# Kernel tuning notes

Hardware: AMD Instinct MI355X
Metric: run time of the kernel (lower is better)

Reference implementation:

```python
import jax, jax.numpy as jnp
import numpy as np

WS = 7            # window_size
HEADS = 12
HEAD_DIM = 32
DIM = 384
INNER = HEADS * HEAD_DIM
DISP = WS // 2    # displacement for shifted windows


def _rel_indices():
    idx = np.array([[x, y] for x in range(WS) for y in range(WS)])  # (49,2)
    d = idx[None, :, :] - idx[:, None, :] + WS - 1                   # (49,49,2), values in [0, 2*WS-2]
    return d


def _masks():
    # upper/lower mask (applied to last row of windows)
    ul = np.zeros((WS * WS, WS * WS), np.float32)
    ul[-DISP * WS:, :-DISP * WS] = -np.inf
    ul[:-DISP * WS, -DISP * WS:] = -np.inf
    # left/right mask (applied to last column of windows)
    lr = np.zeros((WS, WS, WS, WS), np.float32)
    lr[:, -DISP:, :, :-DISP] = -np.inf
    lr[:, :-DISP, :, -DISP:] = -np.inf
    lr = lr.reshape(WS * WS, WS * WS)
    return ul, lr


_RI = _rel_indices()
_UL, _LR = _masks()


def setup_inputs() -> dict:
    key = jax.random.key(0)
    k1, k2, k3, k4, k5 = jax.random.split(key, 5)
    b, H, W = 32, 56, 56
    x = jax.random.normal(k1, (b, H, W, DIM), jnp.float32)
    w_qkv = jax.random.normal(k2, (DIM, 3 * INNER), jnp.float32) * (DIM ** -0.5)
    pos_emb = jax.random.normal(k3, (2 * WS - 1, 2 * WS - 1), jnp.float32)
    w_out = jax.random.normal(k4, (INNER, DIM), jnp.float32) * (INNER ** -0.5)
    b_out = jax.random.normal(k5, (DIM,), jnp.float32)
    return {"x": x, "w_qkv": w_qkv, "pos_emb": pos_emb, "w_out": w_out, "b_out": b_out}


def reference(x, w_qkv, pos_emb, w_out, b_out):
    b, H, W, _ = x.shape
    nwh, nww = H // WS, W // WS
    # cyclic shift
    x = jnp.roll(x, (-DISP, -DISP), (1, 2))
    qkv = x @ w_qkv                                     # [b,H,W,3*INNER]
    q, k, v = jnp.split(qkv, 3, axis=-1)

    def to_win(t):
        # [b,H,W,INNER] -> [b, heads, n_windows, WS*WS, head_dim]
        t = t.reshape(b, nwh, WS, nww, WS, HEADS, HEAD_DIM)
        return t.transpose(0, 5, 1, 3, 2, 4, 6).reshape(b, HEADS, nwh * nww, WS * WS, HEAD_DIM)

    q, k, v = map(to_win, (q, k, v))
    dots = jnp.einsum('bhwid,bhwjd->bhwij', q, k) * (HEAD_DIM ** -0.5)
    # relative position bias gather
    dots = dots + pos_emb[_RI[:, :, 0], _RI[:, :, 1]]
    # shifted-window masks: last row of windows and last column of windows
    dots = dots.at[:, :, -nww:].add(jnp.asarray(_UL))
    dots = dots.at[:, :, nww - 1::nww].add(jnp.asarray(_LR))
    attn = jax.nn.softmax(dots, axis=-1)
    out = jnp.einsum('bhwij,bhwjd->bhwid', attn, v)
    # windows back to image layout
    out = out.reshape(b, HEADS, nwh, nww, WS, WS, HEAD_DIM)
    out = out.transpose(0, 2, 4, 3, 5, 1, 6).reshape(b, H, W, INNER)
    out = out @ w_out + b_out
    return jnp.roll(out, (DISP, DISP), (1, 2))
```

## Files before the change

### kernel.cpp

```cpp
#include <hip/hip_runtime.h>

typedef __attribute__((ext_vector_type(8))) short short8;
typedef __attribute__((ext_vector_type(4))) int int4v;
typedef __attribute__((ext_vector_type(4))) float f32x4;

#define MFMA(a, b, c) __builtin_amdgcn_mfma_f32_16x16x32_bf16(a, b, c, 0, 0, 0)
#define SCALE 0.17677669529663687f

__device__ __forceinline__ short f2bf(float f) {
  union { float f; unsigned u; } v;
  v.f = f;
  unsigned r = v.u + 0x7fffu + ((v.u >> 16) & 1u);
  return (short)(r >> 16);
}

__device__ __forceinline__ unsigned cvt_pk(float lo, float hi) {
  unsigned r;
  asm("v_cvt_pk_bf16_f32 %0, %1, %2" : "=v"(r) : "v"(lo), "v"(hi));
  return r;
}

#define XS_STR 424
#define VT_OFF 0
#define Q_OFF  16384
#define K_OFF  28928
#define AO_STR 392

__global__ void prep_weights(const float* __restrict__ wqkv,
                             const float* __restrict__ wout,
                             short* __restrict__ wqkvT,
                             short* __restrict__ woutT) {
  int i = blockIdx.x * 256 + threadIdx.x;
  if (i < 1152 * 384) {
    int n = i / 384, k = i - (i / 384) * 384;
    float w = wqkv[k * 1152 + n];
    if (n < 384) w *= SCALE;
    wqkvT[i] = f2bf(w);
  }
  if (i < 384 * 384) {
    int n = i / 384, k = i - (i / 384) * 384;
    woutT[i] = f2bf(wout[k * 384 + n]);
  }
}

__global__ void prep_bias(const float* __restrict__ pe, float* __restrict__ btabT) {
  int id = blockIdx.x * 256 + threadIdx.x;
  if (id >= 16384) return;
  int t = id >> 12;
  int i = (id >> 6) & 63;
  int j = id & 63;
  float v;
  if (i < 49 && j < 49) {
    int ai = i / 7, bi = i - ai * 7, aj = j / 7, bj = j - aj * 7;
    v = pe[(aj - ai + 6) * 13 + (bj - bi + 6)];
    if ((t & 1) && ((i >= 28) != (j >= 28))) v = -1e30f;
    if ((t & 2) && ((bi >= 4) != (bj >= 4))) v = -1e30f;
  } else if (j < 49) {
    v = 0.f;
  } else {
    v = -1e30f;
  }
  btabT[((t * 64 + i) * 16 + (j & 15)) * 4 + (j >> 4)] = v;
}

#define GEMM_STEP(BUF)                                                        \
  {                                                                           \
    short8 a0 = *(const short8*)(pA[0] + k * 32);                             \
    short8 a1 = *(const short8*)(pA[1] + k * 32);                             \
    short8 a2 = *(const short8*)(pA[2] + k * 32);                             \
    short8 a3 = *(const short8*)(pA[3] + k * 32);                             \
    acc[0][0] = MFMA(a0, BUF[0], acc[0][0]);                                  \
    acc[1][0] = MFMA(a1, BUF[0], acc[1][0]);                                  \
    acc[2][0] = MFMA(a2, BUF[0], acc[2][0]);                                  \
    acc[3][0] = MFMA(a3, BUF[0], acc[3][0]);                                  \
    acc[0][1] = MFMA(a0, BUF[1], acc[0][1]);                                  \
    acc[1][1] = MFMA(a1, BUF[1], acc[1][1]);                                  \
    acc[2][1] = MFMA(a2, BUF[1], acc[2][1]);                                  \
    acc[3][1] = MFMA(a3, BUF[1], acc[3][1]);                                  \
    acc[0][2] = MFMA(a0, BUF[2], acc[0][2]);                                  \
    acc[1][2] = MFMA(a1, BUF[2], acc[1][2]);                                  \
    acc[2][2] = MFMA(a2, BUF[2], acc[2][2]);                                  \
    acc[3][2] = MFMA(a3, BUF[2], acc[3][2]);                                  \
  }

#define GEMM_PIPELINE()                                                       \
  _Pragma("unroll")                                                           \
  for (int n = 0; n < 3; ++n) bA[n] = *(const short8*)(pB[n]);                \
  _Pragma("unroll")                                                           \
  for (int n = 0; n < 3; ++n) bB[n] = *(const short8*)(pB[n] + 32);           \
  _Pragma("unroll")                                                           \
  for (int k = 0; k < 12; ++k) {                                              \
    if (k + 2 < 12) {                                                         \
      const int off = (k + 2) * 32;                                           \
      if (k % 3 == 0) {                                                       \
        _Pragma("unroll")                                                     \
        for (int n = 0; n < 3; ++n) bC[n] = *(const short8*)(pB[n] + off);    \
      } else if (k % 3 == 1) {                                                \
        _Pragma("unroll")                                                     \
        for (int n = 0; n < 3; ++n) bA[n] = *(const short8*)(pB[n] + off);    \
      } else {                                                                \
        _Pragma("unroll")                                                     \
        for (int n = 0; n < 3; ++n) bB[n] = *(const short8*)(pB[n] + off);    \
      }                                                                       \
    }                                                                         \
    if (k % 3 == 0) GEMM_STEP(bA)                                             \
    else if (k % 3 == 1) GEMM_STEP(bB)                                        \
    else GEMM_STEP(bC)                                                        \
  }

__global__ __launch_bounds__(512, 4) void swin_qkv_attn(
    const float* __restrict__ x, const short* __restrict__ wqkvT,
    const float* __restrict__ btabT, short* __restrict__ aout) {

  __shared__ short smemA[49 * XS_STR];
  char* smc = (char*)smemA;

  const int tid = threadIdx.x;
  const int lane = tid & 63;
  const int wv = tid >> 6;
  const int l15 = lane & 15;
  const int lhi = lane >> 4;

  const int bid = blockIdx.x;
  const int sw = (bid & 7) * 768 + (bid >> 3);
  const int g = sw - (sw / 3) * 3;
  const int bw = sw / 3;
  const int batch = bw >> 6;
  const int win = bw & 63;
  const int wy = win >> 3, wx = win & 7;

  const size_t xbase = (size_t)batch * (56 * 56 * 384);
  const f32x4 zf = {0.f, 0.f, 0.f, 0.f};

  {
    const int tok = tid >> 3;
    const int sub = tid & 7;
    if (tok < 49) {
      int iy = (tok * 37) >> 8;
      int ix = tok - iy * 7;
      int rr = wy * 7 + iy + 3; if (rr >= 56) rr -= 56;
      int cc = wx * 7 + ix + 3; if (cc >= 56) cc -= 56;
      const float* xp = x + xbase + (size_t)(rr * 56 + cc) * 384;
#pragma unroll
      for (int j = 0; j < 6; ++j) {
        const int c8 = (sub + 8 * j) * 8;
        const float4 fa = *(const float4*)(xp + c8);
        const float4 fb = *(const float4*)(xp + c8 + 4);
        int4v p;
        p.x = (int)cvt_pk(fa.x, fa.y);
        p.y = (int)cvt_pk(fa.z, fa.w);
        p.z = (int)cvt_pk(fb.x, fb.y);
        p.w = (int)cvt_pk(fb.z, fb.w);
        *(int4v*)(&smemA[tok * XS_STR + c8]) = p;
      }
    }
  }
  __syncthreads();

  f32x4 acc[4][3];
  const int n0 = wv * 48;
  {
    const short* pB[3];
#pragma unroll
    for (int n = 0; n < 3; ++n) {
      const int c0 = n0 + n * 16;
      const int seg = c0 >> 7;
      const int hloc = (c0 >> 5) & 3;
      const int wrow = seg * 384 + (g * 4 + hloc) * 32 + (c0 & 31);
      pB[n] = wqkvT + (size_t)(wrow + l15) * 384 + lhi * 8;
    }
#pragma unroll
    for (int m = 0; m < 4; ++m)
#pragma unroll
      for (int n = 0; n < 3; ++n) acc[m][n] = zf;

    const short* pA[4];
#pragma unroll
    for (int m = 0; m < 4; ++m) {
      int row = m * 16 + l15;
      int rc = row < 49 ? row : 48;
      pA[m] = &smemA[rc * XS_STR + lhi * 8];
    }

    short8 bA[3], bB[3], bC[3];
    GEMM_PIPELINE()
  }
  __syncthreads();

  {
#pragma unroll
    for (int n = 0; n < 3; ++n) {
      const int c0 = n0 + n * 16;
      if (c0 < 256) {
#pragma unroll
        for (int m = 0; m < 4; ++m)
#pragma unroll
          for (int r = 0; r < 4; ++r) {
            const int row = m * 16 + lhi * 4 + r;
            if (row < 49) {
              const int f = c0 + l15;
              const int base = (f < 128) ? Q_OFF : K_OFF;
              const int fo = (f & 127) * 2;
              *(short*)(smc + base + row * 256 + (fo ^ ((row & 7) << 4))) =
                  f2bf(acc[m][n][r]);
            }
          }
      } else {
        const int d = c0 - 256 + l15;
        char* vrow = smc + VT_OFF + d * 128;
        const int dx = (d & 7) << 4;
#pragma unroll
        for (int m = 0; m < 4; ++m)
#pragma unroll
          for (int r = 0; r < 4; r += 2) {
            const int row = m * 16 + lhi * 4 + r;
            const unsigned pk = cvt_pk(acc[m][n][r], acc[m][n][r + 1]);
            *(unsigned*)(vrow + ((2 * row) ^ dx)) = pk;
          }
      }
    }
  }
  __syncthreads();

  {
    const int hl = wv >> 1;
    const int mh = wv & 1;
    const int tt = (wy == 7 ? 1 : 0) | (wx == 7 ? 2 : 0);

    f32x4 bb[2][4];
#pragma unroll
    for (int mi = 0; mi < 2; ++mi)
#pragma unroll
      for (int r = 0; r < 4; ++r) {
        const int i = mh * 32 + mi * 16 + lhi * 4 + r;
        bb[mi][r] = *(const f32x4*)(&btabT[((tt * 64 + i) * 16 + l15) * 4]);
      }

    short8 qa[2];
#pragma unroll
    for (int mi = 0; mi < 2; ++mi) {
      int row = mh * 32 + mi * 16 + l15;
      int rc = row < 49 ? row : 48;
      qa[mi] = *(const short8*)(smc + Q_OFF + rc * 256 +
                                ((hl * 64 + lhi * 16) ^ ((rc & 7) << 4)));
    }
    f32x4 s[2][4];
#pragma unroll
    for (int nt = 0; nt < 4; ++nt) {
      int jr = nt * 16 + l15;
      int jc = jr < 49 ? jr : 48;
      short8 kb = *(const short8*)(smc + K_OFF + jc * 256 +
                                   ((hl * 64 + lhi * 16) ^ ((jc & 7) << 4)));
#pragma unroll
      for (int mi = 0; mi < 2; ++mi) s[mi][nt] = MFMA(qa[mi], kb, zf);
    }

#pragma unroll
    for (int mi = 0; mi < 2; ++mi)
#pragma unroll
      for (int r = 0; r < 4; ++r)
#pragma unroll
        for (int nt = 0; nt < 4; ++nt)
          s[mi][nt][r] += bb[mi][r][nt];

#pragma unroll
    for (int mi = 0; mi < 2; ++mi)
#pragma unroll
      for (int r = 0; r < 4; ++r) {
        float mx = fmaxf(fmaxf(s[mi][0][r], s[mi][1][r]),
                         fmaxf(s[mi][2][r], s[mi][3][r]));
        mx = fmaxf(mx, __shfl_xor(mx, 1));
        mx = fmaxf(mx, __shfl_xor(mx, 2));
        mx = fmaxf(mx, __shfl_xor(mx, 4));
        mx = fmaxf(mx, __shfl_xor(mx, 8));
        float p0 = __expf(s[mi][0][r] - mx);
        float p1 = __expf(s[mi][1][r] - mx);
        float p2 = __expf(s[mi][2][r] - mx);
        float p3 = __expf(s[mi][3][r] - mx);
        float sum = p0 + p1 + p2 + p3;
        sum += __shfl_xor(sum, 1);
        sum += __shfl_xor(sum, 2);
        sum += __shfl_xor(sum, 4);
        sum += __shfl_xor(sum, 8);
        const float inv = __builtin_amdgcn_rcpf(sum);
        s[mi][0][r] = p0 * inv;
        s[mi][1][r] = p1 * inv;
        s[mi][2][r] = p2 * inv;
        s[mi][3][r] = p3 * inv;
      }

    short8 vb[2][2];
#pragma unroll
    for (int ks = 0; ks < 2; ++ks)
#pragma unroll
      for (int n2 = 0; n2 < 2; ++n2) {
        const int dg = hl * 32 + n2 * 16 + l15;
        vb[ks][n2] = *(const short8*)(smc + VT_OFF + dg * 128 +
                                      ((ks * 64 + lhi * 16) ^ ((dg & 7) << 4)));
      }

    __syncthreads();

    char* Pb = smc + Q_OFF + wv * 2304;
    f32x4 O[2][2];
#pragma unroll
    for (int mi = 0; mi < 2; ++mi) {
#pragma unroll
      for (int r = 0; r < 4; ++r) {
        const int rowl = lhi * 4 + r;
        short* pr = (short*)(Pb + rowl * 144);
        pr[ 0 + l15] = f2bf(s[mi][0][r]);
        pr[16 + l15] = f2bf(s[mi][1][r]);
        pr[32 + l15] = f2bf(s[mi][2][r]);
        pr[48 + l15] = f2bf(s[mi][3][r]);
      }
      const short8 pa0 = *(const short8*)(Pb + l15 * 144 +  0 + lhi * 16);
      const short8 pa1 = *(const short8*)(Pb + l15 * 144 + 64 + lhi * 16);
      O[mi][0] = MFMA(pa0, vb[0][0], zf);
      O[mi][1] = MFMA(pa0, vb[0][1], zf);
      O[mi][0] = MFMA(pa1, vb[1][0], O[mi][0]);
      O[mi][1] = MFMA(pa1, vb[1][1], O[mi][1]);
    }

    short* ab = aout + (size_t)bw * (49 * 384) + (g * 4 + hl) * 32;
#pragma unroll
    for (int mi = 0; mi < 2; ++mi)
#pragma unroll
      for (int n2 = 0; n2 < 2; ++n2)
#pragma unroll
        for (int r = 0; r < 4; ++r) {
          int row = mh * 32 + mi * 16 + lhi * 4 + r;
          if (row < 49) ab[row * 384 + n2 * 16 + l15] = f2bf(O[mi][n2][r]);
        }
  }
}

__global__ __launch_bounds__(512, 4) void swin_outproj(
    const short* __restrict__ aout, const short* __restrict__ woutT,
    const float* __restrict__ bout, float* __restrict__ out) {

  __shared__ short ao[49 * AO_STR];

  const int tid = threadIdx.x;
  const int lane = tid & 63;
  const int wv = tid >> 6;
  const int l15 = lane & 15;
  const int lhi = lane >> 4;

  const int bw = blockIdx.x;
  const int batch = bw >> 6;
  const int win = bw & 63;
  const int wy = win >> 3, wx = win & 7;

  const size_t xbase = (size_t)batch * (56 * 56 * 384);
  const f32x4 zf = {0.f, 0.f, 0.f, 0.f};

  const short* abg = aout + (size_t)bw * (49 * 384);
  for (int t = tid; t < 49 * 48; t += 512) {
    int row = t / 48;
    int seg = t - row * 48;
    *(short8*)(&ao[row * AO_STR + seg * 8]) = *(const short8*)(&abg[row * 384 + seg * 8]);
  }
  __syncthreads();

  {
    const int n0 = wv * 48;
    f32x4 acc[4][3];
#pragma unroll
    for (int m = 0; m < 4; ++m)
#pragma unroll
      for (int n = 0; n < 3; ++n) acc[m][n] = zf;

    const short* pB[3];
#pragma unroll
    for (int n = 0; n < 3; ++n)
      pB[n] = woutT + (size_t)(n0 + n * 16 + l15) * 384 + lhi * 8;

    const short* pA[4];
#pragma unroll
    for (int m = 0; m < 4; ++m) {
      int row = m * 16 + l15;
      int rc = row < 49 ? row : 48;
      pA[m] = &ao[rc * AO_STR + lhi * 8];
    }

    short8 bA[3], bB[3], bC[3];
    GEMM_PIPELINE()

    float bo[3];
#pragma unroll
    for (int n = 0; n < 3; ++n) bo[n] = bout[n0 + n * 16 + l15];

#pragma unroll
    for (int m = 0; m < 4; ++m)
#pragma unroll
      for (int r = 0; r < 4; ++r) {
        const int row = m * 16 + lhi * 4 + r;
        if (row < 49) {
          int iy = (row * 37) >> 8, ix = row - iy * 7;
          int rr = wy * 7 + iy + 3; if (rr >= 56) rr -= 56;
          int cc = wx * 7 + ix + 3; if (cc >= 56) cc -= 56;
          float* dst = out + xbase + (size_t)(rr * 56 + cc) * 384 + n0;
#pragma unroll
          for (int n = 0; n < 3; ++n) dst[n * 16 + l15] = acc[m][n][r] + bo[n];
        }
      }
  }
}

extern "C" void kernel_launch(void* const* d_in, const int* in_sizes, int n_in,
                              void* d_out, int out_size, void* d_ws, size_t ws_size,
                              hipStream_t stream) {
  const float* x    = (const float*)d_in[0];
  const float* wqkv = (const float*)d_in[1];
  const float* pos  = (const float*)d_in[2];
  const float* wout = (const float*)d_in[3];
  const float* bo   = (const float*)d_in[4];

  char* ws = (char*)d_ws;
  short* wqkvT = (short*)ws;                         ws += 1152 * 384 * 2;
  short* woutT = (short*)ws;                         ws += 384 * 384 * 2;
  float* btabT = (float*)ws;                         ws += 4 * 64 * 16 * 4 * 4;
  short* aoutg = (short*)ws;

  prep_weights<<<1728, 256, 0, stream>>>(wqkv, wout, wqkvT, woutT);
  prep_bias<<<64, 256, 0, stream>>>(pos, btabT);
  swin_qkv_attn<<<6144, 512, 0, stream>>>(x, wqkvT, btabT, aoutg);
  swin_outproj<<<2048, 512, 0, stream>>>(aoutg, woutT, bo, (float*)d_out);
}
```

Before: 375.4 us.

## Load activations directly from global into MFMA operands, skipping LDS staging

Removes the shared-memory staging of the 49-token input tile and its barrier. Each wave now loads fp32 activations from global memory, converts them to bf16 in registers and feeds MFMA directly. The triple-buffered B prefetch pipeline is replaced with a simple unrolled loop. This cuts LDS footprint and a sync, at the cost of redundant global reads across waves and less latency hiding.

```diff
diff --git a/kernel.cpp b/kernel.cpp
--- a/kernel.cpp
+++ b/kernel.cpp
@@ -20,7 +20,6 @@
   return r;
 }
 
-#define XS_STR 424
 #define VT_OFF 0
 #define Q_OFF  16384
 #define K_OFF  28928
@@ -112,8 +111,8 @@
     const float* __restrict__ x, const short* __restrict__ wqkvT,
     const float* __restrict__ btabT, short* __restrict__ aout) {
 
-  __shared__ short smemA[49 * XS_STR];
-  char* smc = (char*)smemA;
+  __shared__ short8 arena[2592];
+  char* smc = (char*)arena;
 
   const int tid = threadIdx.x;
   const int lane = tid & 63;
@@ -132,31 +131,6 @@
   const size_t xbase = (size_t)batch * (56 * 56 * 384);
   const f32x4 zf = {0.f, 0.f, 0.f, 0.f};
 
-  {
-    const int tok = tid >> 3;
-    const int sub = tid & 7;
-    if (tok < 49) {
-      int iy = (tok * 37) >> 8;
-      int ix = tok - iy * 7;
-      int rr = wy * 7 + iy + 3; if (rr >= 56) rr -= 56;
-      int cc = wx * 7 + ix + 3; if (cc >= 56) cc -= 56;
-      const float* xp = x + xbase + (size_t)(rr * 56 + cc) * 384;
-#pragma unroll
-      for (int j = 0; j < 6; ++j) {
-        const int c8 = (sub + 8 * j) * 8;
-        const float4 fa = *(const float4*)(xp + c8);
-        const float4 fb = *(const float4*)(xp + c8 + 4);
-        int4v p;
-        p.x = (int)cvt_pk(fa.x, fa.y);
-        p.y = (int)cvt_pk(fa.z, fa.w);
-        p.z = (int)cvt_pk(fb.x, fb.y);
-        p.w = (int)cvt_pk(fb.z, fb.w);
-        *(int4v*)(&smemA[tok * XS_STR + c8]) = p;
-      }
-    }
-  }
-  __syncthreads();
-
   f32x4 acc[4][3];
   const int n0 = wv * 48;
   {
@@ -174,18 +148,39 @@
 #pragma unroll
       for (int n = 0; n < 3; ++n) acc[m][n] = zf;
 
-    const short* pA[4];
+    const float* pAg[4];
 #pragma unroll
     for (int m = 0; m < 4; ++m) {
       int row = m * 16 + l15;
-      int rc = row < 49 ? row : 48;
-      pA[m] = &smemA[rc * XS_STR + lhi * 8];
-    }
-
-    short8 bA[3], bB[3], bC[3];
-    GEMM_PIPELINE()
-  }
-  __syncthreads();
+      int tok = row < 49 ? row : 48;
+      int iy = (tok * 37) >> 8;
+      int ix = tok - iy * 7;
+      int rr = wy * 7 + iy + 3; if (rr >= 56) rr -= 56;
+      int cc = wx * 7 + ix + 3; if (cc >= 56) cc -= 56;
+      pAg[m] = x + xbase + (size_t)(rr * 56 + cc) * 384 + lhi * 8;
+    }
+
+#pragma unroll
+    for (int k = 0; k < 12; ++k) {
+      const short8 b0 = *(const short8*)(pB[0] + k * 32);
+      const short8 b1 = *(const short8*)(pB[1] + k * 32);
+      const short8 b2 = *(const short8*)(pB[2] + k * 32);
+#pragma unroll
+      for (int m = 0; m < 4; ++m) {
+        const float4 fa = *(const float4*)(pAg[m] + k * 32);
+        const float4 fb = *(const float4*)(pAg[m] + k * 32 + 4);
+        int4v p;
+        p.x = (int)cvt_pk(fa.x, fa.y);
+        p.y = (int)cvt_pk(fa.z, fa.w);
+        p.z = (int)cvt_pk(fb.x, fb.y);
+        p.w = (int)cvt_pk(fb.z, fb.w);
+        union { int4v i; short8 s; } u; u.i = p;
+        acc[m][0] = MFMA(u.s, b0, acc[m][0]);
+        acc[m][1] = MFMA(u.s, b1, acc[m][1]);
+        acc[m][2] = MFMA(u.s, b2, acc[m][2]);
+      }
+    }
+  }
 
   {
 #pragma unroll
```

After: 764.0 us. +103.5%, slower.

## Give X panel its own LDS region and drop two block-wide barriers

Applied to the files above, without the earlier changes.

The bf16 X panel moves into a dedicated LDS region after the Q/K/V area, so the QKV GEMM results can be written without first waiting for all waves to finish reading X. The P staging buffer also moves to that region, which lets V be read inside the PV loop and removes the barrier before P is written. The triple-buffered B-register pipeline is replaced by a simple unrolled k-loop that loads B directly. The cost is a larger LDS footprint per block, which may lower occupancy, and a loss of explicit software prefetch of weights.

```diff
diff --git a/kernel.cpp b/kernel.cpp
--- a/kernel.cpp
+++ b/kernel.cpp
@@ -20,10 +20,11 @@
   return r;
 }
 
-#define XS_STR 424
 #define VT_OFF 0
 #define Q_OFF  16384
 #define K_OFF  28928
+#define XP_OFF 41472
+#define XS_STR 408
 #define AO_STR 392
 
 __global__ void prep_weights(const float* __restrict__ wqkv,
@@ -112,8 +113,9 @@
     const float* __restrict__ x, const short* __restrict__ wqkvT,
     const float* __restrict__ btabT, short* __restrict__ aout) {
 
-  __shared__ short smemA[49 * XS_STR];
-  char* smc = (char*)smemA;
+  __shared__ short8 smem[5091];
+  char* smc = (char*)smem;
+  short* xpan = (short*)(smc + XP_OFF);
 
   const int tid = threadIdx.x;
   const int lane = tid & 63;
@@ -151,7 +153,7 @@
         p.y = (int)cvt_pk(fa.z, fa.w);
         p.z = (int)cvt_pk(fb.x, fb.y);
         p.w = (int)cvt_pk(fb.z, fb.w);
-        *(int4v*)(&smemA[tok * XS_STR + c8]) = p;
+        *(int4v*)(&xpan[tok * XS_STR + c8]) = p;
       }
     }
   }
@@ -179,13 +181,23 @@
     for (int m = 0; m < 4; ++m) {
       int row = m * 16 + l15;
       int rc = row < 49 ? row : 48;
-      pA[m] = &smemA[rc * XS_STR + lhi * 8];
-    }
-
-    short8 bA[3], bB[3], bC[3];
-    GEMM_PIPELINE()
-  }
-  __syncthreads();
+      pA[m] = &xpan[rc * XS_STR + lhi * 8];
+    }
+
+#pragma unroll
+    for (int k = 0; k < 12; ++k) {
+      const short8 b0 = *(const short8*)(pB[0] + k * 32);
+      const short8 b1 = *(const short8*)(pB[1] + k * 32);
+      const short8 b2 = *(const short8*)(pB[2] + k * 32);
+#pragma unroll
+      for (int m = 0; m < 4; ++m) {
+        const short8 a = *(const short8*)(pA[m] + k * 32);
+        acc[m][0] = MFMA(a, b0, acc[m][0]);
+        acc[m][1] = MFMA(a, b1, acc[m][1]);
+        acc[m][2] = MFMA(a, b2, acc[m][2]);
+      }
+    }
+  }
 
   {
 #pragma unroll
@@ -289,19 +301,7 @@
         s[mi][3][r] = p3 * inv;
       }
 
-    short8 vb[2][2];
-#pragma unroll
-    for (int ks = 0; ks < 2; ++ks)
-#pragma unroll
-      for (int n2 = 0; n2 < 2; ++n2) {
-        const int dg = hl * 32 + n2 * 16 + l15;
-        vb[ks][n2] = *(const short8*)(smc + VT_OFF + dg * 128 +
-                                      ((ks * 64 + lhi * 16) ^ ((dg & 7) << 4)));
-      }
-
-    __syncthreads();
-
-    char* Pb = smc + Q_OFF + wv * 2304;
+    char* Pb = smc + XP_OFF + wv * 2304;
     f32x4 O[2][2];
 #pragma unroll
     for (int mi = 0; mi < 2; ++mi) {
@@ -316,10 +316,16 @@
       }
       const short8 pa0 = *(const short8*)(Pb + l15 * 144 +  0 + lhi * 16);
       const short8 pa1 = *(const short8*)(Pb + l15 * 144 + 64 + lhi * 16);
-      O[mi][0] = MFMA(pa0, vb[0][0], zf);
-      O[mi][1] = MFMA(pa0, vb[0][1], zf);
-      O[mi][0] = MFMA(pa1, vb[1][0], O[mi][0]);
-      O[mi][1] = MFMA(pa1, vb[1][1], O[mi][1]);
+#pragma unroll
+      for (int n2 = 0; n2 < 2; ++n2) {
+        const int dg = hl * 32 + n2 * 16 + l15;
+        const short8 v0 = *(const short8*)(smc + VT_OFF + dg * 128 +
+                              ((lhi * 16) ^ ((dg & 7) << 4)));
+        const short8 v1 = *(const short8*)(smc + VT_OFF + dg * 128 +
+                              ((64 + lhi * 16) ^ ((dg & 7) << 4)));
+        O[mi][n2] = MFMA(pa0, v0, zf);
+        O[mi][n2] = MFMA(pa1, v1, O[mi][n2]);
+      }
     }
 
     short* ab = aout + (size_t)bw * (49 * 384) + (g * 4 + hl) * 32;
```

Measured after the change: 360.6 us. 4.0% less time.
